# Kernel tuning notes

Measured on AMD Instinct MI355X. Metric: run time of the kernel, lower is better.

Reference implementation:

```python
import jax, jax.numpy as jnp
import numpy as np
import math

B, S, N_UNITS, D_K = 8, 2048, 1024, 512


def setup_inputs() -> dict:
    key = jax.random.key(0)
    ks = jax.random.split(key, 8)
    scale = 1.0 / math.sqrt(N_UNITS)
    query = jax.random.normal(ks[0], (B, S, N_UNITS), dtype=jnp.float32)
    k_in = jax.random.normal(ks[1], (B, S, N_UNITS), dtype=jnp.float32)
    v_in = jax.random.normal(ks[2], (B, S, N_UNITS), dtype=jnp.float32)
    # custom multiplicative mask: causal lower-triangular, broadcast over batch
    mask = jnp.broadcast_to(jnp.tril(jnp.ones((S, S), dtype=jnp.float32)), (B, S, S))
    Wq = jax.random.normal(ks[3], (N_UNITS, D_K), dtype=jnp.float32) * scale
    Wk = jax.random.normal(ks[4], (N_UNITS, D_K), dtype=jnp.float32) * scale
    Wv = jax.random.normal(ks[5], (N_UNITS, D_K), dtype=jnp.float32) * scale
    bq = jnp.zeros((D_K,), dtype=jnp.float32)
    bk = jnp.zeros((D_K,), dtype=jnp.float32)
    bv = jnp.zeros((D_K,), dtype=jnp.float32)
    return {"query": query, "key": k_in, "value": v_in, "mask": mask,
            "Wq": Wq, "bq": bq, "Wk": Wk, "bk": bk, "Wv": Wv, "bv": bv}


def reference(query, key, value, mask, Wq, bq, Wk, bk, Wv, bv):
    d_k = Wq.shape[-1]
    Q = jnp.einsum('bsn,nd->bsd', query, Wq) + bq  # [B,S,Dk]
    K = jnp.einsum('bsn,nd->bsd', key, Wk) + bk
    V = jnp.einsum('bsn,nd->bsd', value, Wv) + bv
    # scores [B,S,S]
    x_hat = jnp.einsum('bqd,bkd->bqk', Q, K) / jnp.sqrt(jnp.float32(d_k))
    # custom multiplicative mask: x*mask - 1e9*(1-mask)
    x_hat_masked = x_hat * mask - 1e9 * (1.0 - mask)
    attn = jax.nn.softmax(x_hat_masked, axis=-1)
    # dropout = 0.0 (eval mode) -> identity
    out = jnp.einsum('bqk,bkd->bqd', attn, V)
    return out
```

## Files before the change

kernel.cpp:

```cpp
#include <hip/hip_runtime.h>

typedef __bf16 bf16_t;
typedef __attribute__((ext_vector_type(4))) __bf16 bf16x4;
typedef __attribute__((ext_vector_type(8))) __bf16 bf16x8;
typedef __attribute__((ext_vector_type(4))) float f32x4;

#define B_    8
#define S_    2048
#define NU    1024
#define DK    512
#define MROWS (B_ * S_)
#define PBATCH (128 * 128 * 136)

#define WAITVM(N) asm volatile("s_waitcnt vmcnt(" #N ")" ::: "memory")
#define WAITLG    asm volatile("s_waitcnt lgkmcnt(0)" ::: "memory")
#define BAR       asm volatile("s_barrier" ::: "memory")

__device__ __forceinline__ f32x4 mfma16(bf16x8 a, bf16x8 b, f32x4 c) {
  return __builtin_amdgcn_mfma_f32_16x16x32_bf16(a, b, c, 0, 0, 0);
}

__device__ __forceinline__ void async_load16(const void* g, void* l) {
  __builtin_amdgcn_global_load_lds(
      (const __attribute__((address_space(1))) unsigned int*)g,
      (__attribute__((address_space(3))) unsigned int*)l, 16, 0, 0);
}

__device__ __forceinline__ bf16x8 cvt8(f32x4 x0, f32x4 x1) {
  bf16x8 r;
#pragma unroll
  for (int j = 0; j < 4; ++j) { r[j] = (bf16_t)x0[j]; r[j + 4] = (bf16_t)x1[j]; }
  return r;
}

__device__ __forceinline__ void stage_tile(const bf16_t* __restrict__ src,
                                           int rstride, bf16_t* dst, int k0,
                                           int tid) {
#pragma unroll
  for (int j = 0; j < 2; ++j) {
    const int g = j * 256 + tid;
    const int ln = g >> 3, c = g & 7;
    const int cs = c ^ (ln & 7);
    const int srow = 2 * ln + (cs >> 2);
    async_load16(src + (size_t)srow * rstride + k0 + (cs & 3) * 8, dst + g * 8);
  }
}

__device__ __forceinline__ void stage_tile64(const bf16_t* __restrict__ src,
                                             int rstride, bf16_t* dst, int k0,
                                             int tid) {
  const int ln = tid >> 3, c = tid & 7;
  const int cs = c ^ (ln & 7);
  const int srow = 2 * ln + (cs >> 2);
  async_load16(src + (size_t)srow * rstride + k0 + (cs & 3) * 8, dst + tid * 8);
}

__device__ __forceinline__ void stage_tile_f32(const float* __restrict__ src,
                                               int rstride, float* dst, int k0,
                                               int tid) {
#pragma unroll
  for (int j = 0; j < 4; ++j) {
    const int g = j * 256 + tid;
    const int row = g >> 3, c = g & 7;
    const int cs = c ^ (row & 7);
    async_load16(src + (size_t)row * rstride + k0 + (cs << 2), dst + g * 4);
  }
}

__device__ __forceinline__ bf16x8 frag(const bf16_t* buf, int row, int q) {
  const int ln = row >> 1;
  const int cp = (((row & 1) << 2) | q) ^ (ln & 7);
  return *(const bf16x8*)(buf + ln * 64 + cp * 8);
}

__global__ __launch_bounds__(256) void transpose_w_kernel(
    const float* __restrict__ Wq, const float* __restrict__ Wk,
    const float* __restrict__ Wv, bf16_t* __restrict__ Wt) {
  const float* W = (blockIdx.z == 0) ? Wq : (blockIdx.z == 1) ? Wk : Wv;
  bf16_t* Wo = Wt + (size_t)blockIdx.z * DK * NU;
  __shared__ float tile[32][33];
  const int t = threadIdx.x;
  const int r = t >> 5, c = t & 31;
  const int kbase = blockIdx.y * 32, nbase = blockIdx.x * 32;
#pragma unroll
  for (int i = 0; i < 4; ++i)
    tile[r + i * 8][c] = W[(size_t)(kbase + r + i * 8) * DK + nbase + c];
  __syncthreads();
#pragma unroll
  for (int i = 0; i < 4; ++i)
    Wo[(size_t)(nbase + r + i * 8) * NU + kbase + c] = (bf16_t)tile[c][r + i * 8];
}

__global__ __launch_bounds__(256, 2) void xw3_gemm_kernel(
    const float* __restrict__ q_in, const float* __restrict__ k_in,
    const float* __restrict__ v_in, const bf16_t* __restrict__ Wt,
    const float* __restrict__ bq, const float* __restrict__ bk,
    const float* __restrict__ bv, bf16_t* __restrict__ Qo,
    bf16_t* __restrict__ Ko, bf16_t* __restrict__ Vt) {
  const int bx = blockIdx.x;
  const int z = bx >> 9;
  const int t = bx & 511;
  const int m0 = (t & 127) * 128;
  const int n0 = (t >> 7) * 128;
  const float* X = (z == 0) ? q_in : (z == 1) ? k_in : v_in;
  const float* bias = (z == 0) ? bq : (z == 1) ? bk : bv;

  const int tid = threadIdx.x;
  const int wave = tid >> 6, lane = tid & 63;
  const int l16 = lane & 15, quad = lane >> 4;
  const int wm = (wave >> 1) * 64, wn = (wave & 1) * 64;

  __shared__ __align__(16) unsigned char smem[65536];
  bf16_t* ldsA = (bf16_t*)smem;
  bf16_t* ldsB = (bf16_t*)(smem + 32768);

  const float* Ag = X + (size_t)m0 * NU;
  const bf16_t* Bg = Wt + (size_t)z * DK * NU + (size_t)n0 * NU;

  int g0 = 2 * tid, g1 = 2 * tid + 1;
  const int cs0 = (g0 & 7) ^ ((g0 >> 3) & 7);
  const int cs1 = (g1 & 7) ^ ((g1 >> 3) & 7);
  const int sr0 = 2 * (g0 >> 3) + (cs0 >> 2), c40 = cs0 & 3;
  const int sr1 = 2 * (g1 >> 3) + (cs1 >> 2), c41 = cs1 & 3;
  const float* ap0 = Ag + (size_t)sr0 * NU + c40 * 8;
  const float* ap1 = Ag + (size_t)sr1 * NU + c41 * 8;

#define XW_A_LOAD(S, K0)                                                      \
  f32x4 xl##S##0 = *(const f32x4*)(ap0 + (K0));                               \
  f32x4 xl##S##1 = *(const f32x4*)(ap0 + (K0) + 4);                           \
  f32x4 xl##S##2 = *(const f32x4*)(ap1 + (K0));                               \
  f32x4 xl##S##3 = *(const f32x4*)(ap1 + (K0) + 4);
#define XW_A_WRITE(S, BUFE)                                                   \
  *(bf16x8*)&ldsA[(BUFE) + g0 * 8] = cvt8(xl##S##0, xl##S##1);                \
  *(bf16x8*)&ldsA[(BUFE) + g1 * 8] = cvt8(xl##S##2, xl##S##3);

  f32x4 acc[4][4] = {};

  {
    XW_A_LOAD(0, 0)
    XW_A_LOAD(1, 32)
    XW_A_LOAD(2, 64)
    XW_A_LOAD(3, 96)
    stage_tile(Bg, NU, ldsB, 0, tid);
    stage_tile(Bg, NU, ldsB + 4096, 32, tid);
    stage_tile(Bg, NU, ldsB + 8192, 64, tid);
    stage_tile(Bg, NU, ldsB + 12288, 96, tid);
    XW_A_WRITE(0, 0)
    XW_A_WRITE(1, 4096)
    XW_A_WRITE(2, 8192)
    XW_A_WRITE(3, 12288)
    WAITVM(0);
    WAITLG;
    BAR;
  }

  const int NS = 32;
  for (int j = 0; j < NS / 2; ++j) {
    const int ks2 = 2 * j;
    const int base = (j & 1) * 8192;
    bf16x8 af[2][4], bfr[2][4];
#pragma unroll
    for (int s = 0; s < 2; ++s)
#pragma unroll
      for (int i = 0; i < 4; ++i) {
        af[s][i] = frag(ldsA + base + s * 4096, wm + i * 16 + l16, quad);
        bfr[s][i] = frag(ldsB + base + s * 4096, wn + i * 16 + l16, quad);
      }
    WAITLG;
    BAR;
    const bool more = (ks2 + 4) < NS;
    if (more) {
      const int k4 = (ks2 + 4) * 32;
      XW_A_LOAD(4, k4)
      XW_A_LOAD(5, k4 + 32)
      stage_tile(Bg, NU, ldsB + base, k4, tid);
      stage_tile(Bg, NU, ldsB + base + 4096, k4 + 32, tid);
      __builtin_amdgcn_s_setprio(1);
#pragma unroll
      for (int s = 0; s < 2; ++s)
#pragma unroll
        for (int i = 0; i < 4; ++i)
#pragma unroll
          for (int jj = 0; jj < 4; ++jj)
            acc[i][jj] = mfma16(af[s][i], bfr[s][jj], acc[i][jj]);
      __builtin_amdgcn_s_setprio(0);
      WAITVM(4);
      XW_A_WRITE(4, base)
      XW_A_WRITE(5, base + 4096)
    } else {
      __builtin_amdgcn_s_setprio(1);
#pragma unroll
      for (int s = 0; s < 2; ++s)
#pragma unroll
        for (int i = 0; i < 4; ++i)
#pragma unroll
          for (int jj = 0; jj < 4; ++jj)
            acc[i][jj] = mfma16(af[s][i], bfr[s][jj], acc[i][jj]);
      __builtin_amdgcn_s_setprio(0);
      WAITVM(0);
    }
    WAITLG;
    BAR;
  }

  if (z != 2) {
    bf16_t* Out = (z == 0) ? Qo : Ko;
#pragma unroll
    for (int j = 0; j < 4; ++j) {
      const int cn = n0 + wn + j * 16 + l16;
      const float bz = bias[cn];
#pragma unroll
      for (int i = 0; i < 4; ++i) {
        const int rm = m0 + wm + i * 16 + quad * 4;
#pragma unroll
        for (int r = 0; r < 4; ++r)
          Out[(size_t)(rm + r) * DK + cn] = (bf16_t)(acc[i][j][r] + bz);
      }
    }
  } else {
    bf16_t* Ts = (bf16_t*)smem;
    BAR;
#pragma unroll
    for (int j = 0; j < 4; ++j) {
      const int cnl = wn + j * 16 + l16;
      const float bz = bias[n0 + cnl];
#pragma unroll
      for (int i = 0; i < 4; ++i) {
#pragma unroll
        for (int r = 0; r < 4; ++r) {
          Ts[cnl * 136 + wm + quad * 16 + r * 4 + i] =
              (bf16_t)(acc[i][j][r] + bz);
        }
      }
    }
    WAITLG; BAR;
    const int bb2 = m0 >> 11, sl = m0 & 2047;
    const int row = tid >> 1, half = tid & 1;
    bf16_t* dst = Vt + ((size_t)bb2 * DK + n0 + row) * S_ + sl + half * 64;
    const bf16_t* sp = &Ts[row * 136 + half * 64];
#pragma unroll
    for (int k = 0; k < 8; ++k)
      *(bf16x8*)(dst + k * 8) = *(const bf16x8*)(sp + k * 8);
  }
#undef XW_A_LOAD
#undef XW_A_WRITE
}

__global__ __launch_bounds__(256, 2) void qk_p_kernel(
    const bf16_t* __restrict__ Q, const bf16_t* __restrict__ K,
    bf16_t* __restrict__ P, float* __restrict__ Lp) {
  const int bx = blockIdx.x;
  const int b = bx & 7;
  const int t = bx >> 3;
  int mt = 0;
  while (((mt + 1) * (mt + 2)) / 2 <= t) ++mt;
  const int nt = t - (mt * (mt + 1)) / 2;
  const int klen = (mt + 1) * 128;

  const int tid = threadIdx.x;
  const int wave = tid >> 6, lane = tid & 63;
  const int l16 = lane & 15, quad = lane >> 4;
  const int wm = (wave >> 1) * 64, wn = (wave & 1) * 64;

  __shared__ __align__(16) unsigned char smem[65536];
  bf16_t* ldsA = (bf16_t*)smem;
  bf16_t* ldsB = (bf16_t*)(smem + 32768);

  const bf16_t* Ag = Q + (size_t)(b * S_ + mt * 128) * DK;
  const bf16_t* Bg = K + (size_t)(b * S_ + nt * 128) * DK;

  f32x4 acc[4][4] = {};

  stage_tile(Ag, DK, ldsA, 0, tid);
  stage_tile(Bg, DK, ldsB, 0, tid);
  stage_tile(Ag, DK, ldsA + 4096, 32, tid);
  stage_tile(Bg, DK, ldsB + 4096, 32, tid);
  stage_tile(Ag, DK, ldsA + 8192, 64, tid);
  stage_tile(Bg, DK, ldsB + 8192, 64, tid);
  stage_tile(Ag, DK, ldsA + 12288, 96, tid);
  stage_tile(Bg, DK, ldsB + 12288, 96, tid);
  WAITVM(8);
  BAR;

  const int NS = 16;
  for (int j = 0; j < NS / 2; ++j) {
    const int ks2 = 2 * j;
    const int base = (j & 1) * 8192;
    bf16x8 af[2][4], bfr[2][4];
#pragma unroll
    for (int s = 0; s < 2; ++s)
#pragma unroll
      for (int i = 0; i < 4; ++i) {
        af[s][i] = frag(ldsA + base + s * 4096, wm + i * 16 + l16, quad);
        bfr[s][i] = frag(ldsB + base + s * 4096, wn + i * 16 + l16, quad);
      }
    WAITLG;
    BAR;
    const bool more = (ks2 + 4) < NS;
    if (more) {
      const int k4 = (ks2 + 4) * 32;
      stage_tile(Ag, DK, ldsA + base, k4, tid);
      stage_tile(Bg, DK, ldsB + base, k4, tid);
      stage_tile(Ag, DK, ldsA + base + 4096, k4 + 32, tid);
      stage_tile(Bg, DK, ldsB + base + 4096, k4 + 32, tid);
    }
    __builtin_amdgcn_s_setprio(1);
#pragma unroll
    for (int s = 0; s < 2; ++s)
#pragma unroll
      for (int i = 0; i < 4; ++i)
#pragma unroll
        for (int jj = 0; jj < 4; ++jj)
          acc[i][jj] = mfma16(af[s][i], bfr[s][jj], acc[i][jj]);
    __builtin_amdgcn_s_setprio(0);
    if (more) { WAITVM(8); } else { WAITVM(0); }
    BAR;
  }

  const float scale = 0.04419417382415922f;
  bf16_t* Pt = P + (size_t)b * PBATCH + (size_t)8192 * mt * (mt + 1);
  float* Lph = Lp + ((size_t)(b * 136 + t) * 2 + (wn >> 6)) * 128;
#pragma unroll
  for (int i = 0; i < 4; ++i) {
#pragma unroll
    for (int r = 0; r < 4; ++r) {
      const int lrow = wm + i * 16 + quad * 4 + r;
      const int srow = mt * 128 + lrow;
      float rsum = 0.f;
      bf16x4 pk;
#pragma unroll
      for (int j = 0; j < 4; ++j) {
        const int scol = nt * 128 + wn + j * 16 + l16;
        const float p =
            (scol > srow) ? 0.f : __expf(acc[i][j][r] * scale - 10.0f);
        rsum += p;
        pk[j] = (bf16_t)p;
      }
      *(bf16x4*)&Pt[(size_t)lrow * klen + nt * 128 + wn + l16 * 4] = pk;
#pragma unroll
      for (int off = 8; off >= 1; off >>= 1)
        rsum += __shfl_xor(rsum, off, 64);
      if (l16 == 0) Lph[lrow] = rsum;
    }
  }
}

__global__ __launch_bounds__(256) void lred_kernel(const float* __restrict__ Lp,
                                                   float* __restrict__ L) {
  const int row = blockIdx.x * 256 + threadIdx.x;
  const int b = row >> 11;
  const int wi = row & 2047;
  const int mt = wi >> 7;
  const int lrow = wi & 127;
  const float* lp =
      Lp + ((size_t)(b * 136 + (mt * (mt + 1)) / 2) * 2) * 128 + lrow;
  float s = 0.f;
  for (int n = 0; n <= mt; ++n) s += lp[n * 256] + lp[n * 256 + 128];
  L[row] = s;
}

__global__ __launch_bounds__(256, 3) void pv_kernel(
    const bf16_t* __restrict__ P, const bf16_t* __restrict__ Vt,
    const float* __restrict__ L, float* __restrict__ Out) {
  const int bx = blockIdx.x;
  const int low = bx & 63;
  const int b = low & 7;
  const int d0 = ((low >> 3) & 3) * 128;
  const int half = (low >> 5) & 1;
  const int g = bx >> 6;
  const int q2 = g >> 2, rb = g & 3;
  const int mt = (q2 == 0) ? 15 - 2 * rb
               : (q2 == 1) ? 2 * rb
               : (q2 == 2) ? 14 - 2 * rb
                           : 1 + 2 * rb;
  const int klen = (mt + 1) * 128;
  const int NS = (mt + 1) * 4;

  const int tid = threadIdx.x;
  const int wave = tid >> 6, lane = tid & 63;
  const int l16 = lane & 15, quad = lane >> 4;
  const int wm = (wave >> 1) * 32, wn = (wave & 1) * 64;

  __shared__ __align__(16) unsigned char smem[49152];
  bf16_t* ldsA = (bf16_t*)smem;
  bf16_t* ldsB = (bf16_t*)(smem + 16384);

  const bf16_t* Ag = P + (size_t)b * PBATCH + (size_t)8192 * mt * (mt + 1) +
                     (size_t)(half * 64) * klen;
  const bf16_t* Bg = Vt + ((size_t)b * DK + d0) * S_;

  f32x4 acc[2][4] = {};

  stage_tile64(Ag, klen, ldsA, 0, tid);
  stage_tile(Bg, S_, ldsB, 0, tid);
  stage_tile64(Ag, klen, ldsA + 2048, 32, tid);
  stage_tile(Bg, S_, ldsB + 4096, 32, tid);
  stage_tile64(Ag, klen, ldsA + 4096, 64, tid);
  stage_tile(Bg, S_, ldsB + 8192, 64, tid);
  stage_tile64(Ag, klen, ldsA + 6144, 96, tid);
  stage_tile(Bg, S_, ldsB + 12288, 96, tid);
  WAITVM(6);
  BAR;

  for (int j = 0; j < NS / 2; ++j) {
    const int ks2 = 2 * j;
    const int baseA = (j & 1) * 4096;
    const int baseB = (j & 1) * 8192;
    bf16x8 af[2][2], bfr[2][4];
#pragma unroll
    for (int s = 0; s < 2; ++s) {
#pragma unroll
      for (int i = 0; i < 2; ++i)
        af[s][i] = frag(ldsA + baseA + s * 2048, wm + i * 16 + l16, quad);
#pragma unroll
      for (int i = 0; i < 4; ++i)
        bfr[s][i] = frag(ldsB + baseB + s * 4096, wn + i * 16 + l16, quad);
    }
    WAITLG;
    BAR;
    const bool more = (ks2 + 4) < NS;
    if (more) {
      const int k4 = (ks2 + 4) * 32;
      stage_tile64(Ag, klen, ldsA + baseA, k4, tid);
      stage_tile(Bg, S_, ldsB + baseB, k4, tid);
      stage_tile64(Ag, klen, ldsA + baseA + 2048, k4 + 32, tid);
      stage_tile(Bg, S_, ldsB + baseB + 4096, k4 + 32, tid);
    }
    __builtin_amdgcn_s_setprio(1);
#pragma unroll
    for (int s = 0; s < 2; ++s)
#pragma unroll
      for (int i = 0; i < 2; ++i)
#pragma unroll
        for (int jj = 0; jj < 4; ++jj)
          acc[i][jj] = mfma16(af[s][i], bfr[s][jj], acc[i][jj]);
    __builtin_amdgcn_s_setprio(0);
    if (more) { WAITVM(6); } else { WAITVM(0); }
    BAR;
  }

  const int m0 = b * S_ + mt * 128 + half * 64;
#pragma unroll
  for (int i = 0; i < 2; ++i) {
#pragma unroll
    for (int r = 0; r < 4; ++r) {
      const int lr = wm + i * 16 + quad * 4 + r;
      const float inv = 1.0f / L[m0 + lr];
      float* orow = Out + (size_t)(m0 + lr) * DK + d0;
#pragma unroll
      for (int j = 0; j < 4; ++j)
        orow[wn + j * 16 + l16] = acc[i][j][r] * inv;
    }
  }
}

extern "C" void kernel_launch(void* const* d_in, const int* in_sizes, int n_in,
                              void* d_out, int out_size, void* d_ws, size_t ws_size,
                              hipStream_t stream) {
  const float* query = (const float*)d_in[0];
  const float* key_i = (const float*)d_in[1];
  const float* value = (const float*)d_in[2];
  const float* Wq = (const float*)d_in[4];
  const float* bq = (const float*)d_in[5];
  const float* Wk = (const float*)d_in[6];
  const float* bk = (const float*)d_in[7];
  const float* Wv = (const float*)d_in[8];
  const float* bv = (const float*)d_in[9];
  float* out = (float*)d_out;

  bf16_t* Wt = (bf16_t*)d_ws;
  bf16_t* Qw = Wt + (size_t)3 * DK * NU;
  bf16_t* Kw = Qw + (size_t)MROWS * DK;
  bf16_t* Vw = Kw + (size_t)MROWS * DK;
  bf16_t* Pw = Vw + (size_t)MROWS * DK;
  float* Lpw = (float*)(Pw + (size_t)B_ * PBATCH);
  float* Lw = Lpw + (size_t)B_ * 136 * 2 * 128;

  transpose_w_kernel<<<dim3(16, 32, 3), 256, 0, stream>>>(Wq, Wk, Wv, Wt);
  xw3_gemm_kernel<<<1536, 256, 0, stream>>>(query, key_i, value, Wt, bq, bk,
                                            bv, Qw, Kw, Vw);
  qk_p_kernel<<<1088, 256, 0, stream>>>(Qw, Kw, Pw, Lpw);
  lred_kernel<<<64, 256, 0, stream>>>(Lpw, Lw);
  pv_kernel<<<1024, 256, 0, stream>>>(Pw, Vw, Lw, out);
}
```

Before: 426.5 us.

## Switch QK and PV GEMM pipelines to triple-buffered single-stage LDS ring

```diff
diff --git a/kernel.cpp b/kernel.cpp
--- a/kernel.cpp
+++ b/kernel.cpp
@@ -53,18 +53,6 @@
   const int cs = c ^ (ln & 7);
   const int srow = 2 * ln + (cs >> 2);
   async_load16(src + (size_t)srow * rstride + k0 + (cs & 3) * 8, dst + tid * 8);
-}
-
-__device__ __forceinline__ void stage_tile_f32(const float* __restrict__ src,
-                                               int rstride, float* dst, int k0,
-                                               int tid) {
-#pragma unroll
-  for (int j = 0; j < 4; ++j) {
-    const int g = j * 256 + tid;
-    const int row = g >> 3, c = g & 7;
-    const int cs = c ^ (row & 7);
-    async_load16(src + (size_t)row * rstride + k0 + (cs << 2), dst + g * 4);
-  }
 }
 
 __device__ __forceinline__ bf16x8 frag(const bf16_t* buf, int row, int q) {
@@ -246,7 +234,7 @@
 #undef XW_A_WRITE
 }
 
-__global__ __launch_bounds__(256, 2) void qk_p_kernel(
+__global__ __launch_bounds__(256, 3) void qk_p_kernel(
     const bf16_t* __restrict__ Q, const bf16_t* __restrict__ K,
     bf16_t* __restrict__ P, float* __restrict__ Lp) {
   const int bx = blockIdx.x;
@@ -262,9 +250,9 @@
   const int l16 = lane & 15, quad = lane >> 4;
   const int wm = (wave >> 1) * 64, wn = (wave & 1) * 64;
 
-  __shared__ __align__(16) unsigned char smem[65536];
+  __shared__ __align__(16) unsigned char smem[49152];
   bf16_t* ldsA = (bf16_t*)smem;
-  bf16_t* ldsB = (bf16_t*)(smem + 32768);
+  bf16_t* ldsB = (bf16_t*)(smem + 24576);
 
   const bf16_t* Ag = Q + (size_t)(b * S_ + mt * 128) * DK;
   const bf16_t* Bg = K + (size_t)(b * S_ + nt * 128) * DK;
@@ -277,43 +265,35 @@
   stage_tile(Bg, DK, ldsB + 4096, 32, tid);
   stage_tile(Ag, DK, ldsA + 8192, 64, tid);
   stage_tile(Bg, DK, ldsB + 8192, 64, tid);
-  stage_tile(Ag, DK, ldsA + 12288, 96, tid);
-  stage_tile(Bg, DK, ldsB + 12288, 96, tid);
   WAITVM(8);
   BAR;
 
   const int NS = 16;
-  for (int j = 0; j < NS / 2; ++j) {
-    const int ks2 = 2 * j;
-    const int base = (j & 1) * 8192;
-    bf16x8 af[2][4], bfr[2][4];
-#pragma unroll
-    for (int s = 0; s < 2; ++s)
-#pragma unroll
-      for (int i = 0; i < 4; ++i) {
-        af[s][i] = frag(ldsA + base + s * 4096, wm + i * 16 + l16, quad);
-        bfr[s][i] = frag(ldsB + base + s * 4096, wn + i * 16 + l16, quad);
-      }
+#pragma unroll
+  for (int j = 0; j < NS; ++j) {
+    const int cb = (j % 3) * 4096;
+    bf16x8 af[4], bfr[4];
+#pragma unroll
+    for (int i = 0; i < 4; ++i) {
+      af[i] = frag(ldsA + cb, wm + i * 16 + l16, quad);
+      bfr[i] = frag(ldsB + cb, wn + i * 16 + l16, quad);
+    }
     WAITLG;
     BAR;
-    const bool more = (ks2 + 4) < NS;
-    if (more) {
-      const int k4 = (ks2 + 4) * 32;
-      stage_tile(Ag, DK, ldsA + base, k4, tid);
-      stage_tile(Bg, DK, ldsB + base, k4, tid);
-      stage_tile(Ag, DK, ldsA + base + 4096, k4 + 32, tid);
-      stage_tile(Bg, DK, ldsB + base + 4096, k4 + 32, tid);
+    if (j + 3 < NS) {
+      stage_tile(Ag, DK, ldsA + cb, (j + 3) * 32, tid);
+      stage_tile(Bg, DK, ldsB + cb, (j + 3) * 32, tid);
     }
     __builtin_amdgcn_s_setprio(1);
 #pragma unroll
-    for (int s = 0; s < 2; ++s)
-#pragma unroll
-      for (int i = 0; i < 4; ++i)
-#pragma unroll
-        for (int jj = 0; jj < 4; ++jj)
-          acc[i][jj] = mfma16(af[s][i], bfr[s][jj], acc[i][jj]);
+    for (int i = 0; i < 4; ++i)
+#pragma unroll
+      for (int jj = 0; jj < 4; ++jj)
+        acc[i][jj] = mfma16(af[i], bfr[jj], acc[i][jj]);
     __builtin_amdgcn_s_setprio(0);
-    if (more) { WAITVM(8); } else { WAITVM(0); }
+    if (j + 3 < NS) { WAITVM(8); }
+    else if (j + 2 < NS) { WAITVM(4); }
+    else { WAITVM(0); }
     BAR;
   }
 
@@ -359,7 +339,7 @@
   L[row] = s;
 }
 
-__global__ __launch_bounds__(256, 3) void pv_kernel(
+__global__ __launch_bounds__(256, 4) void pv_kernel(
     const bf16_t* __restrict__ P, const bf16_t* __restrict__ Vt,
     const float* __restrict__ L, float* __restrict__ Out) {
   const int bx = blockIdx.x;
@@ -381,9 +361,9 @@
   const int l16 = lane & 15, quad = lane >> 4;
   const int wm = (wave >> 1) * 32, wn = (wave & 1) * 64;
 
-  __shared__ __align__(16) unsigned char smem[49152];
+  __shared__ __align__(16) unsigned char smem[36864];
   bf16_t* ldsA = (bf16_t*)smem;
-  bf16_t* ldsB = (bf16_t*)(smem + 16384);
+  bf16_t* ldsB = (bf16_t*)(smem + 12288);
 
   const bf16_t* Ag = P + (size_t)b * PBATCH + (size_t)8192 * mt * (mt + 1) +
                      (size_t)(half * 64) * klen;
@@ -397,45 +377,35 @@
   stage_tile(Bg, S_, ldsB + 4096, 32, tid);
   stage_tile64(Ag, klen, ldsA + 4096, 64, tid);
   stage_tile(Bg, S_, ldsB + 8192, 64, tid);
-  stage_tile64(Ag, klen, ldsA + 6144, 96, tid);
-  stage_tile(Bg, S_, ldsB + 12288, 96, tid);
   WAITVM(6);
   BAR;
 
-  for (int j = 0; j < NS / 2; ++j) {
-    const int ks2 = 2 * j;
-    const int baseA = (j & 1) * 4096;
-    const int baseB = (j & 1) * 8192;
-    bf16x8 af[2][2], bfr[2][4];
-#pragma unroll
-    for (int s = 0; s < 2; ++s) {
-#pragma unroll
-      for (int i = 0; i < 2; ++i)
-        af[s][i] = frag(ldsA + baseA + s * 2048, wm + i * 16 + l16, quad);
-#pragma unroll
-      for (int i = 0; i < 4; ++i)
-        bfr[s][i] = frag(ldsB + baseB + s * 4096, wn + i * 16 + l16, quad);
-    }
+  for (int j = 0; j < NS; ++j) {
+    const int m3 = j % 3;
+    const int cbA = m3 * 2048, cbB = m3 * 4096;
+    bf16x8 af[2], bfr[4];
+#pragma unroll
+    for (int i = 0; i < 2; ++i)
+      af[i] = frag(ldsA + cbA, wm + i * 16 + l16, quad);
+#pragma unroll
+    for (int i = 0; i < 4; ++i)
+      bfr[i] = frag(ldsB + cbB, wn + i * 16 + l16, quad);
     WAITLG;
     BAR;
-    const bool more = (ks2 + 4) < NS;
-    if (more) {
-      const int k4 = (ks2 + 4) * 32;
-      stage_tile64(Ag, klen, ldsA + baseA, k4, tid);
-      stage_tile(Bg, S_, ldsB + baseB, k4, tid);
-      stage_tile64(Ag, klen, ldsA + baseA + 2048, k4 + 32, tid);
-      stage_tile(Bg, S_, ldsB + baseB + 4096, k4 + 32, tid);
+    if (j + 3 < NS) {
+      stage_tile64(Ag, klen, ldsA + cbA, (j + 3) * 32, tid);
+      stage_tile(Bg, S_, ldsB + cbB, (j + 3) * 32, tid);
     }
     __builtin_amdgcn_s_setprio(1);
 #pragma unroll
-    for (int s = 0; s < 2; ++s)
-#pragma unroll
-      for (int i = 0; i < 2; ++i)
-#pragma unroll
-        for (int jj = 0; jj < 4; ++jj)
-          acc[i][jj] = mfma16(af[s][i], bfr[s][jj], acc[i][jj]);
+    for (int i = 0; i < 2; ++i)
+#pragma unroll
+      for (int jj = 0; jj < 4; ++jj)
+        acc[i][jj] = mfma16(af[i], bfr[jj], acc[i][jj]);
     __builtin_amdgcn_s_setprio(0);
-    if (more) { WAITVM(6); } else { WAITVM(0); }
+    if (j + 3 < NS) { WAITVM(6); }
+    else if (j + 2 < NS) { WAITVM(3); }
+    else { WAITVM(0); }
     BAR;
   }
 
```

After: 425.6 us. No clear change (-0.2%).
